# Kernel tuning notes

Measured on AMD Instinct MI355X. Metric: run time of the kernel, lower is better.

The kernel has to match this reference:

```python
import jax, jax.numpy as jnp
import numpy as np

ALPHA = 0.2  # TF leaky_relu default

def setup_inputs() -> dict:
    key = jax.random.key(0)
    ks = jax.random.split(key, 6)
    B, N, F, D = 2, 8192, 256, 128
    seq = jax.random.normal(ks[0], (B, N, F), dtype=jnp.float32)
    # Conv1D with kernel size 1 == pointwise linear
    Wf = jax.random.normal(ks[1], (F, D), dtype=jnp.float32) * (1.0 / np.sqrt(F))
    w1 = jax.random.normal(ks[2], (D, 1), dtype=jnp.float32) * (1.0 / np.sqrt(D))
    b1 = jnp.zeros((1,), dtype=jnp.float32)
    w2 = jax.random.normal(ks[3], (D, 1), dtype=jnp.float32) * (1.0 / np.sqrt(D))
    b2 = jnp.zeros((1,), dtype=jnp.float32)
    bias = jnp.zeros((D,), dtype=jnp.float32)
    return {"seq": seq, "Wf": Wf, "w1": w1, "b1": b1, "w2": w2, "b2": b2, "bias": bias}

def reference(seq, Wf, w1, b1, w2, b2, bias):
    # seq: [B,N,F] -> seq_fts: [B,N,D]
    seq_fts = jnp.einsum('bnf,fd->bnd', seq, Wf)
    f1 = jnp.einsum('bnd,do->bno', seq_fts, w1) + b1  # [B,N,1]
    f2 = jnp.einsum('bnd,do->bno', seq_fts, w2) + b2  # [B,N,1]
    logits = f1 + jnp.swapaxes(f2, 1, 2)              # [B,N,N] outer-sum
    coefs = jax.nn.softmax(jax.nn.leaky_relu(logits, ALPHA), axis=-1)
    vals = jnp.einsum('bnm,bmd->bnd', coefs, seq_fts) + bias
    return jax.nn.leaky_relu(vals, ALPHA)
```

## Files before the change

kernel.cpp:

```cpp
#include <hip/hip_runtime.h>
#include <cstddef>

#define ALPHA 0.2f
constexpr int B = 2, N = 8192, F = 256, D = 128;
constexpr int M = B * N;
constexpr int NB = 4096;
constexpr int SUB = 128;
constexpr int P = N / SUB;
constexpr int GB = 2;
constexpr int NBB = NB / GB;
constexpr int GSZ = 64;
constexpr int NGRP = NB / GSZ;
constexpr int QROWS = 8;
constexpr int DSL = 4;
constexpr int NSL = D / DSL;
constexpr int BPT = NB / 128;

#define BMIN (-6.0f)
#define BSCALE ((float)NB / 12.0f)
__device__ inline int bucket_of(float x) {
  int g = (int)((x - BMIN) * BSCALE);
  return g < 0 ? 0 : (g > NB - 1 ? NB - 1 : g);
}

__global__ __launch_bounds__(512) void k_gemm(const float* __restrict__ seq,
                                              const float* __restrict__ Wf,
                                              const float* __restrict__ w1,
                                              const float* __restrict__ b1,
                                              const float* __restrict__ w2,
                                              const float* __restrict__ b2,
                                              float* __restrict__ fts,
                                              float* __restrict__ f1,
                                              float* __restrict__ f2) {
  __shared__ float As[32][68];
  __shared__ float Bs[32][128];
  const int m0 = blockIdx.x * 64;
  const int t = threadIdx.x;
  const int colg = t & 31;
  const int rowg = t >> 5;
  float acc[4][4];
#pragma unroll
  for (int r = 0; r < 4; ++r)
#pragma unroll
    for (int c = 0; c < 4; ++c) acc[r][c] = 0.f;

  for (int kc = 0; kc < F; kc += 32) {
    {
      int row = t >> 3, k4 = t & 7;
      const float4 v = *reinterpret_cast<const float4*>(
          &seq[(size_t)(m0 + row) * F + kc + k4 * 4]);
      As[k4 * 4 + 0][row] = v.x; As[k4 * 4 + 1][row] = v.y;
      As[k4 * 4 + 2][row] = v.z; As[k4 * 4 + 3][row] = v.w;
    }
#pragma unroll
    for (int it = 0; it < 2; ++it) {
      int f = t + it * 512;
      int row = f >> 5, c4 = f & 31;
      *reinterpret_cast<float4*>(&Bs[row][c4 * 4]) =
          *reinterpret_cast<const float4*>(&Wf[(size_t)(kc + row) * D + c4 * 4]);
    }
    __syncthreads();
#pragma unroll
    for (int k = 0; k < 32; ++k) {
      const float4 a4 = *reinterpret_cast<const float4*>(&As[k][rowg * 4]);
      const float4 b4 = *reinterpret_cast<const float4*>(&Bs[k][colg * 4]);
      acc[0][0] += a4.x * b4.x; acc[0][1] += a4.x * b4.y; acc[0][2] += a4.x * b4.z; acc[0][3] += a4.x * b4.w;
      acc[1][0] += a4.y * b4.x; acc[1][1] += a4.y * b4.y; acc[1][2] += a4.y * b4.z; acc[1][3] += a4.y * b4.w;
      acc[2][0] += a4.z * b4.x; acc[2][1] += a4.z * b4.y; acc[2][2] += a4.z * b4.z; acc[2][3] += a4.z * b4.w;
      acc[3][0] += a4.w * b4.x; acc[3][1] += a4.w * b4.y; acc[3][2] += a4.w * b4.z; acc[3][3] += a4.w * b4.w;
    }
    __syncthreads();
  }
#pragma unroll
  for (int r = 0; r < 4; ++r) {
    float4 v = {acc[r][0], acc[r][1], acc[r][2], acc[r][3]};
    *reinterpret_cast<float4*>(&fts[(size_t)(m0 + rowg * 4 + r) * D + colg * 4]) = v;
  }
  const float w1v[4] = {w1[colg * 4], w1[colg * 4 + 1], w1[colg * 4 + 2], w1[colg * 4 + 3]};
  const float w2v[4] = {w2[colg * 4], w2[colg * 4 + 1], w2[colg * 4 + 2], w2[colg * 4 + 3]};
  const float b1v = b1[0], b2v = b2[0];
#pragma unroll
  for (int r = 0; r < 4; ++r) {
    float s1 = acc[r][0] * w1v[0] + acc[r][1] * w1v[1] + acc[r][2] * w1v[2] + acc[r][3] * w1v[3];
    float s2 = acc[r][0] * w2v[0] + acc[r][1] * w2v[1] + acc[r][2] * w2v[2] + acc[r][3] * w2v[3];
#pragma unroll
    for (int off = 16; off > 0; off >>= 1) {
      s1 += __shfl_down(s1, off, 32);
      s2 += __shfl_down(s2, off, 32);
    }
    if (colg == 0) {
      const int row = m0 + rowg * 4 + r;
      f1[row] = s1 + b1v;
      f2[row] = s2 + b2v;
    }
  }
}

__global__ __launch_bounds__(128) void k_hist(const float* __restrict__ f2,
                                              int* __restrict__ bid,
                                              int* __restrict__ histcnt) {
  __shared__ int hist[NB];
  const int b = blockIdx.x / P, p = blockIdx.x % P;
  const int t = threadIdx.x;
  for (int i = t; i < NB; i += 128) hist[i] = 0;
  const int j = p * SUB + t;
  float x = f2[b * N + j];
  int g = bucket_of(x);
  bid[b * N + j] = g;
  __syncthreads();
  atomicAdd(&hist[g], 1);
  __syncthreads();
  for (int i = t; i < NB; i += 128)
    histcnt[((size_t)(b * P + p)) * NB + i] = hist[i];
}

__global__ __launch_bounds__(256) void k_sub(const int* __restrict__ histcnt,
                                             int* __restrict__ substart,
                                             int* __restrict__ btot) {
  const int gid = blockIdx.x * 256 + threadIdx.x;
  const int b = gid / NB, g = gid % NB;
  int run = 0;
  for (int pp = 0; pp < P; ++pp) {
    substart[((size_t)(b * P + pp)) * NB + g] = run;
    run += histcnt[((size_t)(b * P + pp)) * NB + g];
  }
  btot[b * NB + g] = run;
}

__global__ __launch_bounds__(128) void k_scat(const float* __restrict__ f2,
                                              const int* __restrict__ bid,
                                              const int* __restrict__ substart,
                                              const int* __restrict__ btot,
                                              int* __restrict__ bstart,
                                              float4* __restrict__ kw,
                                              int* __restrict__ idxs) {
  __shared__ int bstart_lds[NB];
  __shared__ int bids[SUB];
  __shared__ int wsum2[2];
  const int b = blockIdx.x / P, p = blockIdx.x % P;
  const int t = threadIdx.x;
  const int lane = t & 63, wave = t >> 6;
  const size_t bN = (size_t)b * N;

  int c[BPT];
  int loc = 0;
#pragma unroll
  for (int i = 0; i < BPT; ++i) { c[i] = btot[b * NB + t * BPT + i]; loc += c[i]; }
  int incl = loc;
#pragma unroll
  for (int off = 1; off < 64; off <<= 1) {
    int y = __shfl_up(incl, off);
    if (lane >= off) incl += y;
  }
  if (lane == 63) wsum2[wave] = incl;
  __syncthreads();
  if (wave == 1) incl += wsum2[0];
  int excl = incl - loc;
#pragma unroll
  for (int i = 0; i < BPT; ++i) { bstart_lds[t * BPT + i] = excl; excl += c[i]; }
  __syncthreads();
  if (p == 0) {
    for (int i = t; i < NB; i += 128) bstart[b * (NB + 1) + i] = bstart_lds[i];
    if (t == 0) bstart[b * (NB + 1) + NB] = N;
  }

  const int j = p * SUB + t;
  const int g = bid[bN + j];
  bids[t] = g;
  __syncthreads();
  int off = bstart_lds[g] + substart[((size_t)(b * P + p)) * NB + g];
  for (int jj = 0; jj < t; ++jj) off += (bids[jj] == g);
  const float x = f2[bN + j];
  kw[bN + off] = make_float4(x, expf(x), expf(ALPHA * x), 0.f);
  idxs[bN + off] = j;
}

__global__ __launch_bounds__(256) void k_perm(const float* __restrict__ fts,
                                              const int* __restrict__ idxs,
                                              float* __restrict__ fts_s) {
  const int tid = blockIdx.x * 256 + threadIdx.x;
  const int eg = tid >> 5;
  const int q = tid & 31;
  const int b = eg / N;
  const int j = idxs[eg];
  *reinterpret_cast<float4*>(&fts_s[(size_t)eg * D + q * 4]) =
      *reinterpret_cast<const float4*>(&fts[((size_t)b * N + j) * D + q * 4]);
}

__global__ __launch_bounds__(128) void k_bsum(const float* __restrict__ fts_s,
                                              const float4* __restrict__ kw,
                                              const int* __restrict__ bstart,
                                              float* __restrict__ Wp, float* __restrict__ Wn,
                                              float* __restrict__ Cp, float* __restrict__ Cn) {
  const int b = blockIdx.x / NBB, blk = blockIdx.x % NBB;
  const int d = threadIdx.x;
  const int gbase = blk * GB;
  const size_t bN = (size_t)b * N;
  for (int gg = 0; gg < GB; ++gg) {
    const int g = gbase + gg;
    const int e0 = bstart[b * (NB + 1) + g], e1 = bstart[b * (NB + 1) + g + 1];
    float ap = 0.f, an = 0.f, sp = 0.f, sn = 0.f;
    int e = e0;
    for (; e + 4 <= e1; e += 4) {
      const float* vp = &fts_s[(bN + e) * D + d];
      const float v0 = vp[0], v1 = vp[D], v2 = vp[2 * D], v3 = vp[3 * D];
      const float4 k0 = kw[bN + e], k1 = kw[bN + e + 1], k2 = kw[bN + e + 2], k3 = kw[bN + e + 3];
      ap += k0.y * v0 + k1.y * v1 + k2.y * v2 + k3.y * v3;
      an += k0.z * v0 + k1.z * v1 + k2.z * v2 + k3.z * v3;
      sp += k0.y + k1.y + k2.y + k3.y;
      sn += k0.z + k1.z + k2.z + k3.z;
    }
    for (; e < e1; ++e) {
      const float v = fts_s[(bN + e) * D + d];
      const float4 k0 = kw[bN + e];
      ap += k0.y * v; an += k0.z * v; sp += k0.y; sn += k0.z;
    }
    Wp[((size_t)b * NB + g) * D + d] = ap;
    Wn[((size_t)b * NB + g) * D + d] = an;
    if (d == 0) { Cp[b * NB + g] = sp; Cn[b * NB + g] = sn; }
  }
}

__global__ __launch_bounds__(256) void k_scan(const float* __restrict__ Wp, const float* __restrict__ Wn,
                                              const float* __restrict__ Cp, const float* __restrict__ Cn,
                                              float* __restrict__ BPos, float* __restrict__ BNeg,
                                              float* __restrict__ CpB, float* __restrict__ CnB) {
  __shared__ float gp[NGRP][DSL], gn[NGRP][DSL];
  __shared__ float cgp[NGRP], cgn[NGRP];
  const int b = blockIdx.x / NSL, sl = blockIdx.x % NSL;
  const int t = threadIdx.x;
  const int d4 = t & (DSL - 1), grp = t >> 2;
  const int d = sl * DSL + d4;
  const size_t base = (size_t)b * NB;

  float sp = 0.f, sn = 0.f;
  for (int gg = 0; gg < GSZ; ++gg) {
    const int g = grp * GSZ + gg;
    sp += Wp[(base + g) * D + d];
    sn += Wn[(base + g) * D + d];
  }
  gp[grp][d4] = sp; gn[grp][d4] = sn;
  if (sl == 0 && d4 == 0) {
    float cp = 0.f, cn = 0.f;
    for (int gg = 0; gg < GSZ; ++gg) { const int g = grp * GSZ + gg; cp += Cp[base + g]; cn += Cn[base + g]; }
    cgp[grp] = cp; cgn[grp] = cn;
  }
  __syncthreads();

  if (t < DSL) {
    float run = 0.f;
    for (int g2 = 0; g2 < NGRP; ++g2) { const float v = gn[g2][t]; gn[g2][t] = run; run += v; }
  } else if (t < 2 * DSL) {
    const int dd = t - DSL;
    float run = 0.f;
    for (int g2 = NGRP - 1; g2 >= 0; --g2) { const float v = gp[g2][dd]; gp[g2][dd] = run; run += v; }
  } else if (sl == 0 && t == 2 * DSL) {
    float run = 0.f;
    for (int g2 = 0; g2 < NGRP; ++g2) { const float v = cgn[g2]; cgn[g2] = run; run += v; }
  } else if (sl == 0 && t == 2 * DSL + 1) {
    float run = 0.f;
    for (int g2 = NGRP - 1; g2 >= 0; --g2) { const float v = cgp[g2]; cgp[g2] = run; run += v; }
  }
  __syncthreads();

  float runn = gn[grp][d4];
  for (int gg = 0; gg < GSZ; ++gg) {
    const int g = grp * GSZ + gg;
    BNeg[(base + g) * D + d] = runn;
    runn += Wn[(base + g) * D + d];
  }
  float runp = gp[grp][d4];
  for (int gg = GSZ - 1; gg >= 0; --gg) {
    const int g = grp * GSZ + gg;
    BPos[(base + g) * D + d] = runp;
    runp += Wp[(base + g) * D + d];
  }
  if (sl == 0 && d4 == 0) {
    float rn = cgn[grp];
    for (int gg = 0; gg < GSZ; ++gg) { const int g = grp * GSZ + gg; CnB[base + g] = rn; rn += Cn[base + g]; }
    float rp = cgp[grp];
    for (int gg = GSZ - 1; gg >= 0; --gg) { const int g = grp * GSZ + gg; CpB[base + g] = rp; rp += Cp[base + g]; }
  }
}

__global__ __launch_bounds__(256) void k_query(const float* __restrict__ f1,
                                               const float4* __restrict__ kw,
                                               const float* __restrict__ fts_s,
                                               const int* __restrict__ bstart,
                                               const float* __restrict__ BPos, const float* __restrict__ BNeg,
                                               const float* __restrict__ CpB, const float* __restrict__ CnB,
                                               const float* __restrict__ bias,
                                               float* __restrict__ out) {
  const int r = threadIdx.x >> 5;
  const int lane = threadIdx.x & 31;
  const int row = blockIdx.x * QROWS + r;
  const int b = row / N;
  const size_t bN = (size_t)b * N;
  const int d4 = lane * 4;
  const float f1v = f1[row];
  const float th = -f1v;
  const int g = bucket_of(th);
  const int base = bstart[b * (NB + 1) + g];
  const int end  = bstart[b * (NB + 1) + g + 1];
  float4 sn = *reinterpret_cast<const float4*>(&BNeg[((size_t)b * NB + g) * D + d4]);
  float4 sp = *reinterpret_cast<const float4*>(&BPos[((size_t)b * NB + g) * D + d4]);
  float cn = CnB[b * NB + g];
  float cp = CpB[b * NB + g];
  for (int e = base; e < end; ++e) {
    const float4 kwe = kw[bN + e];
    const float4 v = *reinterpret_cast<const float4*>(&fts_s[(bN + e) * D + d4]);
    const bool neg = (kwe.x <= th);
    const float wn = neg ? kwe.z : 0.f;
    const float wp = neg ? 0.f : kwe.y;
    sn.x += wn * v.x; sn.y += wn * v.y; sn.z += wn * v.z; sn.w += wn * v.w;
    sp.x += wp * v.x; sp.y += wp * v.y; sp.z += wp * v.z; sp.w += wp * v.w;
    cn += wn; cp += wp;
  }
  const float wqp = expf(f1v), wqn = expf(ALPHA * f1v);
  const float denom = wqp * cp + wqn * cn;
  const float inv = 1.0f / denom;
  const float4 bi = *reinterpret_cast<const float4*>(&bias[d4]);
  float4 val;
  val.x = (wqp * sp.x + wqn * sn.x) * inv + bi.x;
  val.y = (wqp * sp.y + wqn * sn.y) * inv + bi.y;
  val.z = (wqp * sp.z + wqn * sn.z) * inv + bi.z;
  val.w = (wqp * sp.w + wqn * sn.w) * inv + bi.w;
  val.x = val.x >= 0.f ? val.x : ALPHA * val.x;
  val.y = val.y >= 0.f ? val.y : ALPHA * val.y;
  val.z = val.z >= 0.f ? val.z : ALPHA * val.z;
  val.w = val.w >= 0.f ? val.w : ALPHA * val.w;
  *reinterpret_cast<float4*>(&out[(size_t)row * D + d4]) = val;
}

extern "C" void kernel_launch(void* const* d_in, const int* in_sizes, int n_in,
                              void* d_out, int out_size, void* d_ws, size_t ws_size,
                              hipStream_t stream) {
  const float* seq  = (const float*)d_in[0];
  const float* Wf   = (const float*)d_in[1];
  const float* w1   = (const float*)d_in[2];
  const float* b1   = (const float*)d_in[3];
  const float* w2   = (const float*)d_in[4];
  const float* b2   = (const float*)d_in[5];
  const float* bias = (const float*)d_in[6];
  float* out = (float*)d_out;

  char* ws = (char*)d_ws;
  size_t off = 0;
  auto alloc = [&](size_t bytes) -> void* {
    void* p = ws + off;
    off = (off + bytes + 255) & ~(size_t)255;
    return p;
  };

  float*  fts     = (float*) alloc((size_t)M * D * 4);
  float*  fts_s   = (float*) alloc((size_t)M * D * 4);
  float*  f1      = (float*) alloc((size_t)M * 4);
  float*  f2      = (float*) alloc((size_t)M * 4);
  float4* kw      = (float4*)alloc((size_t)M * 16);
  int*    idxs    = (int*)   alloc((size_t)M * 4);
  int*    bid     = (int*)   alloc((size_t)M * 4);
  int*    histcnt = (int*)   alloc((size_t)B * P * NB * 4);
  int*    substart= (int*)   alloc((size_t)B * P * NB * 4);
  int*    btot    = (int*)   alloc((size_t)B * NB * 4);
  int*    bstart  = (int*)   alloc((size_t)B * (NB + 1) * 4);
  float*  Wp      = (float*) alloc((size_t)B * NB * D * 4);
  float*  Wn      = (float*) alloc((size_t)B * NB * D * 4);
  float*  Cp      = (float*) alloc((size_t)B * NB * 4);
  float*  Cn      = (float*) alloc((size_t)B * NB * 4);
  float*  BPos    = (float*) alloc((size_t)B * NB * D * 4);
  float*  BNeg    = (float*) alloc((size_t)B * NB * D * 4);
  float*  CpB     = (float*) alloc((size_t)B * NB * 4);
  float*  CnB     = (float*) alloc((size_t)B * NB * 4);

  hipLaunchKernelGGL(k_gemm,  dim3(M / 64),          dim3(512), 0, stream, seq, Wf, w1, b1, w2, b2, fts, f1, f2);
  hipLaunchKernelGGL(k_hist,  dim3(B * P),           dim3(128), 0, stream, f2, bid, histcnt);
  hipLaunchKernelGGL(k_sub,   dim3(B * NB / 256),    dim3(256), 0, stream, histcnt, substart, btot);
  hipLaunchKernelGGL(k_scat,  dim3(B * P),           dim3(128), 0, stream, f2, bid, substart, btot, bstart,
                     kw, idxs);
  hipLaunchKernelGGL(k_perm,  dim3(M * D / 4 / 256), dim3(256), 0, stream, fts, idxs, fts_s);
  hipLaunchKernelGGL(k_bsum,  dim3(B * NBB),         dim3(128), 0, stream, fts_s, kw, bstart, Wp, Wn, Cp, Cn);
  hipLaunchKernelGGL(k_scan,  dim3(B * NSL),         dim3(256), 0, stream, Wp, Wn, Cp, Cn, BPos, BNeg, CpB, CnB);
  hipLaunchKernelGGL(k_query, dim3(M / QROWS),       dim3(256), 0, stream, f1, kw, fts_s, bstart,
                     BPos, BNeg, CpB, CnB, bias, out);
}
```

Baseline: 101.3 us.

## Halve bucket count, retile GEMM per wavefront, split f1/f2 into separate kernel

Halves the number of f2 buckets (NB 4096→2048), which shrinks the histogram, bucket-sum and scan work and the intermediate buffers. The GEMM is retiled so each wavefront computes 16 rows by 64 contiguous columns, giving coalesced scalar stores, and the f1/f2 projection moves into its own kernel that re-reads fts. k_scan runs with 128 threads, matching the smaller group count. The extra kernel adds one launch and a full re-read of fts, and coarser buckets push more per-element work into the query's boundary-bucket handling.

```diff
diff --git a/kernel.cpp b/kernel.cpp
--- a/kernel.cpp
+++ b/kernel.cpp
@@ -4,7 +4,7 @@
 #define ALPHA 0.2f
 constexpr int B = 2, N = 8192, F = 256, D = 128;
 constexpr int M = B * N;
-constexpr int NB = 4096;
+constexpr int NB = 2048;
 constexpr int SUB = 128;
 constexpr int P = N / SUB;
 constexpr int GB = 2;
@@ -25,75 +25,74 @@
 
 __global__ __launch_bounds__(512) void k_gemm(const float* __restrict__ seq,
                                               const float* __restrict__ Wf,
+                                              float* __restrict__ fts) {
+  __shared__ float As[32][68];
+  __shared__ float Bs[32][128];
+  const int m0 = blockIdx.x * 64;
+  const int t = threadIdx.x;
+  const int w = t >> 6;
+  const int l = t & 63;
+  const int r0 = (w & 3) * 16;
+  const int c = (w >> 2) * 64 + l;
+  float acc[16];
+#pragma unroll
+  for (int r = 0; r < 16; ++r) acc[r] = 0.f;
+
+  for (int kc = 0; kc < F; kc += 32) {
+    {
+      const int row = t >> 3, k4 = t & 7;
+      const float4 v = *reinterpret_cast<const float4*>(
+          &seq[(size_t)(m0 + row) * F + kc + k4 * 4]);
+      As[k4 * 4 + 0][row] = v.x; As[k4 * 4 + 1][row] = v.y;
+      As[k4 * 4 + 2][row] = v.z; As[k4 * 4 + 3][row] = v.w;
+    }
+#pragma unroll
+    for (int it = 0; it < 2; ++it) {
+      const int f = t + it * 512;
+      const int row = f >> 5, c4 = f & 31;
+      *reinterpret_cast<float4*>(&Bs[row][c4 * 4]) =
+          *reinterpret_cast<const float4*>(&Wf[(size_t)(kc + row) * D + c4 * 4]);
+    }
+    __syncthreads();
+#pragma unroll
+    for (int k = 0; k < 32; ++k) {
+      const float4 a0 = *reinterpret_cast<const float4*>(&As[k][r0 + 0]);
+      const float4 a1 = *reinterpret_cast<const float4*>(&As[k][r0 + 4]);
+      const float4 a2 = *reinterpret_cast<const float4*>(&As[k][r0 + 8]);
+      const float4 a3 = *reinterpret_cast<const float4*>(&As[k][r0 + 12]);
+      const float bv = Bs[k][c];
+      acc[0]  += a0.x * bv; acc[1]  += a0.y * bv; acc[2]  += a0.z * bv; acc[3]  += a0.w * bv;
+      acc[4]  += a1.x * bv; acc[5]  += a1.y * bv; acc[6]  += a1.z * bv; acc[7]  += a1.w * bv;
+      acc[8]  += a2.x * bv; acc[9]  += a2.y * bv; acc[10] += a2.z * bv; acc[11] += a2.w * bv;
+      acc[12] += a3.x * bv; acc[13] += a3.y * bv; acc[14] += a3.z * bv; acc[15] += a3.w * bv;
+    }
+    __syncthreads();
+  }
+#pragma unroll
+  for (int r = 0; r < 16; ++r)
+    fts[(size_t)(m0 + r0 + r) * D + c] = acc[r];
+}
+
+__global__ __launch_bounds__(256) void k_f1f2(const float* __restrict__ fts,
                                               const float* __restrict__ w1,
                                               const float* __restrict__ b1,
                                               const float* __restrict__ w2,
                                               const float* __restrict__ b2,
-                                              float* __restrict__ fts,
                                               float* __restrict__ f1,
                                               float* __restrict__ f2) {
-  __shared__ float As[32][68];
-  __shared__ float Bs[32][128];
-  const int m0 = blockIdx.x * 64;
-  const int t = threadIdx.x;
-  const int colg = t & 31;
-  const int rowg = t >> 5;
-  float acc[4][4];
-#pragma unroll
-  for (int r = 0; r < 4; ++r)
-#pragma unroll
-    for (int c = 0; c < 4; ++c) acc[r][c] = 0.f;
-
-  for (int kc = 0; kc < F; kc += 32) {
-    {
-      int row = t >> 3, k4 = t & 7;
-      const float4 v = *reinterpret_cast<const float4*>(
-          &seq[(size_t)(m0 + row) * F + kc + k4 * 4]);
-      As[k4 * 4 + 0][row] = v.x; As[k4 * 4 + 1][row] = v.y;
-      As[k4 * 4 + 2][row] = v.z; As[k4 * 4 + 3][row] = v.w;
-    }
-#pragma unroll
-    for (int it = 0; it < 2; ++it) {
-      int f = t + it * 512;
-      int row = f >> 5, c4 = f & 31;
-      *reinterpret_cast<float4*>(&Bs[row][c4 * 4]) =
-          *reinterpret_cast<const float4*>(&Wf[(size_t)(kc + row) * D + c4 * 4]);
-    }
-    __syncthreads();
-#pragma unroll
-    for (int k = 0; k < 32; ++k) {
-      const float4 a4 = *reinterpret_cast<const float4*>(&As[k][rowg * 4]);
-      const float4 b4 = *reinterpret_cast<const float4*>(&Bs[k][colg * 4]);
-      acc[0][0] += a4.x * b4.x; acc[0][1] += a4.x * b4.y; acc[0][2] += a4.x * b4.z; acc[0][3] += a4.x * b4.w;
-      acc[1][0] += a4.y * b4.x; acc[1][1] += a4.y * b4.y; acc[1][2] += a4.y * b4.z; acc[1][3] += a4.y * b4.w;
-      acc[2][0] += a4.z * b4.x; acc[2][1] += a4.z * b4.y; acc[2][2] += a4.z * b4.z; acc[2][3] += a4.z * b4.w;
-      acc[3][0] += a4.w * b4.x; acc[3][1] += a4.w * b4.y; acc[3][2] += a4.w * b4.z; acc[3][3] += a4.w * b4.w;
-    }
-    __syncthreads();
-  }
-#pragma unroll
-  for (int r = 0; r < 4; ++r) {
-    float4 v = {acc[r][0], acc[r][1], acc[r][2], acc[r][3]};
-    *reinterpret_cast<float4*>(&fts[(size_t)(m0 + rowg * 4 + r) * D + colg * 4]) = v;
-  }
-  const float w1v[4] = {w1[colg * 4], w1[colg * 4 + 1], w1[colg * 4 + 2], w1[colg * 4 + 3]};
-  const float w2v[4] = {w2[colg * 4], w2[colg * 4 + 1], w2[colg * 4 + 2], w2[colg * 4 + 3]};
-  const float b1v = b1[0], b2v = b2[0];
-#pragma unroll
-  for (int r = 0; r < 4; ++r) {
-    float s1 = acc[r][0] * w1v[0] + acc[r][1] * w1v[1] + acc[r][2] * w1v[2] + acc[r][3] * w1v[3];
-    float s2 = acc[r][0] * w2v[0] + acc[r][1] * w2v[1] + acc[r][2] * w2v[2] + acc[r][3] * w2v[3];
-#pragma unroll
-    for (int off = 16; off > 0; off >>= 1) {
-      s1 += __shfl_down(s1, off, 32);
-      s2 += __shfl_down(s2, off, 32);
-    }
-    if (colg == 0) {
-      const int row = m0 + rowg * 4 + r;
-      f1[row] = s1 + b1v;
-      f2[row] = s2 + b2v;
-    }
-  }
+  const int wid = threadIdx.x >> 6;
+  const int lane = threadIdx.x & 63;
+  const int row = blockIdx.x * 4 + wid;
+  const float* p = &fts[(size_t)row * D];
+  float x0 = p[lane], x1 = p[lane + 64];
+  float d1 = x0 * w1[lane] + x1 * w1[lane + 64];
+  float d2 = x0 * w2[lane] + x1 * w2[lane + 64];
+#pragma unroll
+  for (int off = 32; off > 0; off >>= 1) {
+    d1 += __shfl_down(d1, off);
+    d2 += __shfl_down(d2, off);
+  }
+  if (lane == 0) { f1[row] = d1 + b1[0]; f2[row] = d2 + b2[0]; }
 }
 
 __global__ __launch_bounds__(128) void k_hist(const float* __restrict__ f2,
@@ -221,7 +220,7 @@
   }
 }
 
-__global__ __launch_bounds__(256) void k_scan(const float* __restrict__ Wp, const float* __restrict__ Wn,
+__global__ __launch_bounds__(128) void k_scan(const float* __restrict__ Wp, const float* __restrict__ Wn,
                                               const float* __restrict__ Cp, const float* __restrict__ Cn,
                                               float* __restrict__ BPos, float* __restrict__ BNeg,
                                               float* __restrict__ CpB, float* __restrict__ CnB) {
@@ -372,14 +371,15 @@
   float*  CpB     = (float*) alloc((size_t)B * NB * 4);
   float*  CnB     = (float*) alloc((size_t)B * NB * 4);
 
-  hipLaunchKernelGGL(k_gemm,  dim3(M / 64),          dim3(512), 0, stream, seq, Wf, w1, b1, w2, b2, fts, f1, f2);
+  hipLaunchKernelGGL(k_gemm,  dim3(M / 64),          dim3(512), 0, stream, seq, Wf, fts);
+  hipLaunchKernelGGL(k_f1f2,  dim3(M / 4),           dim3(256), 0, stream, fts, w1, b1, w2, b2, f1, f2);
   hipLaunchKernelGGL(k_hist,  dim3(B * P),           dim3(128), 0, stream, f2, bid, histcnt);
   hipLaunchKernelGGL(k_sub,   dim3(B * NB / 256),    dim3(256), 0, stream, histcnt, substart, btot);
   hipLaunchKernelGGL(k_scat,  dim3(B * P),           dim3(128), 0, stream, f2, bid, substart, btot, bstart,
                      kw, idxs);
   hipLaunchKernelGGL(k_perm,  dim3(M * D / 4 / 256), dim3(256), 0, stream, fts, idxs, fts_s);
   hipLaunchKernelGGL(k_bsum,  dim3(B * NBB),         dim3(128), 0, stream, fts_s, kw, bstart, Wp, Wn, Cp, Cn);
-  hipLaunchKernelGGL(k_scan,  dim3(B * NSL),         dim3(256), 0, stream, Wp, Wn, Cp, Cn, BPos, BNeg, CpB, CnB);
+  hipLaunchKernelGGL(k_scan,  dim3(B * NSL),         dim3(128), 0, stream, Wp, Wn, Cp, Cn, BPos, BNeg, CpB, CnB);
   hipLaunchKernelGGL(k_query, dim3(M / QROWS),       dim3(256), 0, stream, f1, kw, fts_s, bstart,
                      BPos, BNeg, CpB, CnB, bias, out);
 }
```

New measurement: 98.02 us. 3.2% less time.
